# Kernel tuning notes

Hardware: AMD Instinct MI355X
Metric: run time of the kernel (lower is better)

## Reference

```python
import jax, jax.numpy as jnp
import numpy as np

B, T, D = 2, 512, 512
NUM_SCALES, MIN_S, MAX_S = 10, 0.01, 1.0
SCALES_NP = np.logspace(np.log10(MIN_S), np.log10(MAX_S), NUM_SCALES)


def _golay():
    # extended Golay (24,12) generator exactly as in _initialize_golay_code
    G = np.zeros((12, 24), np.float32)
    for i in range(12):
        G[i, i] = 1.0
        for j in range(11):
            G[i, 12 + j] = (i + j) % 2
        G[i, 23] = G[i, :23].sum() % 2
    return jnp.asarray(G)

GOLAY = _golay()  # [12,24]


def setup_inputs() -> dict:
    key = jax.random.key(0)
    ks = jax.random.split(key, 6)
    return {
        'token_ids': jax.random.randint(ks[0], (B, T), 0, 1000000, dtype=jnp.int32),
        'resonances': jax.random.uniform(ks[1], (D,), minval=1.0, maxval=50.0, dtype=jnp.float32),
        'emb_scales': jnp.ones((D,), jnp.float32),
        'emb_shifts': jnp.zeros((D,), jnp.float32),
        'emb_norm': jnp.ones((1,), jnp.float32),
        'scale_weights': jnp.ones((NUM_SCALES,), jnp.float32),
        'fractal_bias': jnp.zeros((1,), jnp.float32),
        'frac_norm': jnp.ones((1,), jnp.float32),
        'W_enc': jax.random.normal(ks[2], (D, 24), jnp.float32) / np.float32(np.sqrt(D)),
        'b_enc': jnp.zeros((24,), jnp.float32),
        'W_dec': jax.random.normal(ks[3], (24, D), jnp.float32) / np.float32(np.sqrt(24)),
        'b_dec': jnp.zeros((D,), jnp.float32),
        'ecc_strength': jnp.full((1,), 0.1, jnp.float32),
        'energy_preservation': jnp.ones((1,), jnp.float32),
    }


def _fractal_dimension(signal, scale_weights, fractal_bias, frac_norm):
    # differentiable box-counting (GenuineFractalAnalyzer.compute_fractal_dimension)
    input_energy = jnp.linalg.norm(signal)
    s = signal.reshape(-1)  # [N]
    s = (s - s.min()) / (s.max() - s.min() + 1e-8)
    counts = []
    for scale_np in SCALES_NP:
        nb = int(round(1.0 / scale_np))  # static per scale: 100 ... 1
        edges = jnp.linspace(0.0, 1.0, nb + 1)
        lo, hi = edges[:-1][:, None], edges[1:][:, None]  # [nb,1]
        # vectorized over boxes instead of python loop over boxes
        in_box = jax.nn.sigmoid(10.0 * (s[None, :] - lo)) * jax.nn.sigmoid(10.0 * (hi - s[None, :]))  # [nb,N]
        occ = in_box.sum(axis=1)  # [nb]
        counts.append(jax.nn.sigmoid(occ - 0.5).sum())
    box_counts = jnp.stack(counts)  # [NUM_SCALES]
    weighted = box_counts * jax.nn.softmax(scale_weights)
    scales = jnp.asarray(SCALES_NP, jnp.float32)
    log_x = jnp.log(1.0 / scales)
    log_y = jnp.log(weighted + 1e-8)
    n = np.float32(NUM_SCALES)
    sx, sy = log_x.sum(), log_y.sum()
    sxy, sx2 = (log_x * log_y).sum(), (log_x ** 2).sum()
    slope = (n * sxy - sx * sy) / (n * sx2 - sx ** 2 + 1e-8)
    fd = jnp.clip(-slope + fractal_bias, 1.0, 2.5)  # [1]
    out_energy = jnp.linalg.norm(fd)
    return fd * frac_norm * input_energy / out_energy


def reference(token_ids, resonances, emb_scales, emb_shifts, emb_norm, scale_weights,
              fractal_bias, frac_norm, W_enc, b_enc, W_dec, b_dec, ecc_strength,
              energy_preservation):
    # --- GenuineEmbedding.batch_encode (vectorized over B,T,D) ---
    token_value = (token_ids % 1000000).astype(jnp.float32) / 1e6  # [B,T]
    pos = jnp.arange(T, dtype=jnp.float32)  # [T]
    angle = resonances[None, None, :] * (token_value[:, :, None] + pos[None, :, None])  # [B,T,D]
    c, sn = jnp.cos(angle), jnp.sin(angle)
    comp = c * (1.0 + sn) + sn * sn
    emb = comp * emb_scales + emb_shifts
    tok_norm = jnp.linalg.norm(emb, axis=-1, keepdims=True)
    emb = jnp.where(tok_norm > 0, emb * emb_norm / tok_norm, emb)

    # --- GenuineLeechLattice.encode_to_lattice ---
    ecc = ecc_strength[0]
    ep = energy_preservation[0]
    e_in = jnp.linalg.norm(emb, axis=-1, keepdims=True)  # b t 1
    proj = emb @ W_enc + b_enc  # [B,T,24]
    golay_enc = jnp.einsum('btl,kl->btk', proj, GOLAY)  # [B,T,12]
    latt = jnp.round(golay_enc / ecc) * ecc
    e_out = jnp.linalg.norm(latt, axis=-1, keepdims=True)
    latt = latt * (e_in / (e_out + 1e-8)) * ep

    # --- GenuineLeechLattice.decode_from_lattice ---
    e_in2 = jnp.linalg.norm(latt, axis=-1, keepdims=True)
    golay_dec = jnp.einsum('btk,kl->btl', latt, GOLAY)  # [B,T,24]
    corrected = jnp.where(jnp.abs(golay_dec) > ecc, golay_dec, 0.0)
    res = corrected @ W_dec + b_dec  # [B,T,D]
    e_out2 = jnp.linalg.norm(res, axis=-1, keepdims=True)
    res = res * (e_in2 / (e_out2 + 1e-8)) * ep

    # --- GenuineFractalAnalyzer on the corrected signal, then modulate ---
    fd = _fractal_dimension(res, scale_weights, fractal_bias, frac_norm)  # [1]
    return res * fd
```

## Files before the change

### kernel.cpp

```cpp
#include <hip/hip_runtime.h>
#include <math.h>

#define NT   1024
#define TT   512
#define DD   512


__device__ __forceinline__ float np_pairwise512(const float* x, int tid) {
    float r = 0.0f;
    if (tid < 32) {
        const int b = tid >> 3, j = tid & 7;
        const float* p = x + 128 * b + j;
        r = p[0];
        #pragma unroll
        for (int i = 1; i < 16; i++) r = __fadd_rn(r, p[8 * i]);
    }
    r = __fadd_rn(r, __shfl_down(r, 1, 64));
    r = __fadd_rn(r, __shfl_down(r, 2, 64));
    r = __fadd_rn(r, __shfl_down(r, 4, 64));
    r = __fadd_rn(r, __shfl_down(r, 8, 64));
    r = __fadd_rn(r, __shfl_down(r, 16, 64));
    return r;
}

__device__ __forceinline__ float np_pairwise12(const float* a) {
    float r = __fadd_rn(__fadd_rn(__fadd_rn(a[0], a[1]), __fadd_rn(a[2], a[3])),
                        __fadd_rn(__fadd_rn(a[4], a[5]), __fadd_rn(a[6], a[7])));
    r = __fadd_rn(r, a[8]);
    r = __fadd_rn(r, a[9]);
    r = __fadd_rn(r, a[10]);
    r = __fadd_rn(r, a[11]);
    return r;
}

__global__ __launch_bounds__(512, 6) void token_kernel(
    const int*   __restrict__ token_ids,
    const float* __restrict__ resonances,
    const float* __restrict__ emb_scales,
    const float* __restrict__ emb_shifts,
    const float* __restrict__ emb_norm,
    const float* __restrict__ W_enc,
    const float* __restrict__ b_enc,
    const float* __restrict__ W_dec,
    const float* __restrict__ b_dec,
    const float* __restrict__ ecc_p,
    const float* __restrict__ ep_p,
    float*       __restrict__ out,
    double*      __restrict__ partials)
{
    const int tok  = blockIdx.x;
    const int t    = tok % TT;
    const int tid  = threadIdx.x;
    const int lane = tid & 63;
    const int wave = tid >> 6;

    __shared__ float  sh_w[DD * 24];
    __shared__ float  sh_e[DD];
    __shared__ float  sh_x[DD];
    __shared__ float  sh_c[24];
    __shared__ float  sh_sc[4];
    __shared__ double sh_red[8];

    {
        const float4* src = (const float4*)W_enc;
        float4*       dst = (float4*)sh_w;
        #pragma unroll
        for (int i = 0; i < 6; i++)
            dst[tid + 512 * i] = src[tid + 512 * i];
    }

    const float ecc   = ecc_p[0];
    const float ep    = ep_p[0];
    const float enorm = emb_norm[0];

    const int   idv  = token_ids[tok];
    const float tv   = __fdiv_rn((float)idv, 1000000.0f);
    const float base = __fadd_rn(tv, (float)t);

    float e0;
    {
        const float a0 = __fmul_rn(resonances[tid], base);
        double s0d, c0d;
        sincos((double)a0, &s0d, &c0d);
        const float s0 = (float)s0d, c0 = (float)c0d;
        const float comp0 = __fadd_rn(__fmul_rn(c0, __fadd_rn(1.0f, s0)), __fmul_rn(s0, s0));
        e0 = __fadd_rn(__fmul_rn(comp0, emb_scales[tid]), emb_shifts[tid]);
    }
    sh_x[tid] = __fmul_rn(e0, e0);
    __syncthreads();

    float ps = np_pairwise512(sh_x, tid);
    if (tid == 0) sh_sc[0] = __fsqrt_rn(ps);
    __syncthreads();
    const float tok_norm = sh_sc[0];
    if (tok_norm > 0.0f)
        e0 = __fdiv_rn(__fmul_rn(e0, enorm), tok_norm);
    sh_e[tid] = e0;
    sh_x[tid] = __fmul_rn(e0, e0);
    __syncthreads();

    ps = np_pairwise512(sh_x, tid);
    const float e_in = __fsqrt_rn(ps);

    if (wave == 0) {
        float p = 0.0f;
        if (lane < 24) {
            float acc = 0.0f;
            #pragma unroll 8
            for (int d = 0; d < DD; d++)
                acc = fmaf(sh_e[d], sh_w[d * 24 + lane], acc);
            p = __fadd_rn(acc, b_enc[lane]);
        }

        float latt = 0.0f;
        {
            const int k = lane;
            float g = p;
            #pragma unroll
            for (int l = 12; l < 23; l++) {
                const float v = __shfl(p, l, 64);
                if ((k + l) & 1) g = __fadd_rn(g, v);
            }
            const float v23 = __shfl(p, 23, 64);
            if (k & 1) g = __fadd_rn(g, v23);
            latt = __fmul_rn(rintf(__fdiv_rn(g, ecc)), ecc);
        }

        float lt[12];
        #pragma unroll
        for (int k = 0; k < 12; k++) lt[k] = __shfl(latt, k, 64);
        float m1;
        {
            float sq[12];
            #pragma unroll
            for (int k = 0; k < 12; k++) sq[k] = __fmul_rn(lt[k], lt[k]);
            const float e_out = __fsqrt_rn(np_pairwise12(sq));
            m1 = __fdiv_rn(e_in, __fadd_rn(e_out, 1e-8f));
        }
        m1 = __shfl(m1, 0, 64);
        float lv[12];
        #pragma unroll
        for (int k = 0; k < 12; k++) lv[k] = __fmul_rn(__fmul_rn(lt[k], m1), ep);
        if (lane == 0) {
            float sq[12];
            #pragma unroll
            for (int k = 0; k < 12; k++) sq[k] = __fmul_rn(lv[k], lv[k]);
            sh_sc[2] = __fsqrt_rn(np_pairwise12(sq));
        }

        if (lane < 24) {
            const int l = lane;
            float g;
            if (l < 12) {
                g = lv[l];
            } else if (l < 23) {
                g = 0.0f;
                #pragma unroll
                for (int k = 0; k < 12; k++)
                    if ((k + l) & 1) g = __fadd_rn(g, lv[k]);
            } else {
                g = 0.0f;
                for (int k = 1; k < 12; k += 2) g = __fadd_rn(g, lv[k]);
            }
            sh_c[l] = (fabsf(g) > ecc) ? g : 0.0f;
        }
    }
    __syncthreads();

    float r0 = 0.0f;
    #pragma unroll
    for (int l = 0; l < 24; l++)
        r0 = fmaf(sh_c[l], W_dec[l * DD + tid], r0);
    r0 = __fadd_rn(r0, b_dec[tid]);
    sh_x[tid] = __fmul_rn(r0, r0);
    __syncthreads();
    ps = np_pairwise512(sh_x, tid);
    if (tid == 0) sh_sc[3] = __fsqrt_rn(ps);
    __syncthreads();

    const float m2 = __fdiv_rn(sh_sc[2], __fadd_rn(sh_sc[3], 1e-8f));
    const float f0 = __fmul_rn(__fmul_rn(r0, m2), ep);
    out[tok * DD + tid] = f0;

    double v4 = (double)f0 * (double)f0;
    for (int off = 32; off > 0; off >>= 1) v4 += __shfl_down(v4, off, 64);
    if (lane == 0) sh_red[wave] = v4;
    __syncthreads();
    if (tid == 0) {
        double s = sh_red[0];
        #pragma unroll
        for (int w = 1; w < 8; w++) s += sh_red[w];
        partials[tok] = s;
    }
}

__global__ __launch_bounds__(256) void scale_kernel(
    float*        __restrict__ out,
    const double* __restrict__ partials,
    const float*  __restrict__ frac_norm)
{
    const int tid = threadIdx.x;
    __shared__ double sh[4];
    __shared__ float sh_factor;
    double s = 0.0;
    #pragma unroll
    for (int i = 0; i < 4; i++) s += partials[tid + 256 * i];
    for (int off = 32; off > 0; off >>= 1) s += __shfl_down(s, off, 64);
    if ((tid & 63) == 0) sh[tid >> 6] = s;
    __syncthreads();
    if (tid == 0)
        sh_factor = (float)((double)frac_norm[0] * sqrt(sh[0] + sh[1] + sh[2] + sh[3]));
    __syncthreads();
    const float factor = sh_factor;

    const int i = blockIdx.x * blockDim.x + tid;
    float4 r = ((const float4*)out)[i];
    r.x = __fmul_rn(r.x, factor);
    r.y = __fmul_rn(r.y, factor);
    r.z = __fmul_rn(r.z, factor);
    r.w = __fmul_rn(r.w, factor);
    ((float4*)out)[i] = r;
}

extern "C" void kernel_launch(void* const* d_in, const int* in_sizes, int n_in,
                              void* d_out, int out_size, void* d_ws, size_t ws_size,
                              hipStream_t stream)
{
    const int*   token_ids  = (const int*)  d_in[0];
    const float* resonances = (const float*)d_in[1];
    const float* emb_scales = (const float*)d_in[2];
    const float* emb_shifts = (const float*)d_in[3];
    const float* emb_norm   = (const float*)d_in[4];
    const float* frac_norm  = (const float*)d_in[7];
    const float* W_enc      = (const float*)d_in[8];
    const float* b_enc      = (const float*)d_in[9];
    const float* W_dec      = (const float*)d_in[10];
    const float* b_dec      = (const float*)d_in[11];
    const float* ecc        = (const float*)d_in[12];
    const float* ep         = (const float*)d_in[13];

    double* partials = (double*)d_ws;

    token_kernel<<<NT, 512, 0, stream>>>(token_ids, resonances, emb_scales, emb_shifts,
                                         emb_norm, W_enc, b_enc, W_dec, b_dec, ecc, ep,
                                         (float*)d_out, partials);
    scale_kernel<<<(NT * DD) / 1024, 256, 0, stream>>>((float*)d_out, partials, frac_norm);
}
```

Measured before the change: 102.9 us.

## Process four tokens per 1024-thread block to share the W_enc LDS tile

Each block now handles four tokens, with 256 threads per token and two embedding dimensions per thread. The 48KB W_enc shared-memory load is amortised over four tokens instead of one, cutting global-to-LDS traffic and the number of block launches fourfold. The cost is one large block per CU, which relies on four concurrent encode waves for latency hiding. The per-token double sum of squares now pairs two elements per thread before the shuffle, which slightly changes the reduction order.

```diff
diff --git a/kernel.cpp b/kernel.cpp
--- a/kernel.cpp
+++ b/kernel.cpp
@@ -6,10 +6,10 @@
 #define DD   512
 
 
-__device__ __forceinline__ float np_pairwise512(const float* x, int tid) {
+__device__ __forceinline__ float np_pairwise512(const float* x, int htid) {
     float r = 0.0f;
-    if (tid < 32) {
-        const int b = tid >> 3, j = tid & 7;
+    if (htid < 32) {
+        const int b = htid >> 3, j = htid & 7;
         const float* p = x + 128 * b + j;
         r = p[0];
         #pragma unroll
@@ -33,7 +33,7 @@
     return r;
 }
 
-__global__ __launch_bounds__(512, 6) void token_kernel(
+__global__ __launch_bounds__(1024, 4) void token_kernel(
     const int*   __restrict__ token_ids,
     const float* __restrict__ resonances,
     const float* __restrict__ emb_scales,
@@ -48,25 +48,27 @@
     float*       __restrict__ out,
     double*      __restrict__ partials)
 {
-    const int tok  = blockIdx.x;
+    const int tid  = threadIdx.x;
+    const int q    = tid >> 8;
+    const int htid = tid & 255;
+    const int tok  = blockIdx.x * 4 + q;
     const int t    = tok % TT;
-    const int tid  = threadIdx.x;
-    const int lane = tid & 63;
-    const int wave = tid >> 6;
+    const int w4   = htid >> 6;
+    const int hlane = htid & 63;
 
     __shared__ float  sh_w[DD * 24];
-    __shared__ float  sh_e[DD];
-    __shared__ float  sh_x[DD];
-    __shared__ float  sh_c[24];
-    __shared__ float  sh_sc[4];
-    __shared__ double sh_red[8];
+    __shared__ float  sh_e[4][DD];
+    __shared__ float  sh_x[4][DD];
+    __shared__ float  sh_c[4][24];
+    __shared__ float  sh_sc[4][4];
+    __shared__ double sh_red[4][4];
 
     {
         const float4* src = (const float4*)W_enc;
         float4*       dst = (float4*)sh_w;
         #pragma unroll
-        for (int i = 0; i < 6; i++)
-            dst[tid + 512 * i] = src[tid + 512 * i];
+        for (int i = 0; i < 3; i++)
+            dst[tid + 1024 * i] = src[tid + 1024 * i];
     }
 
     const float ecc   = ecc_p[0];
@@ -77,44 +79,54 @@
     const float tv   = __fdiv_rn((float)idv, 1000000.0f);
     const float base = __fadd_rn(tv, (float)t);
 
-    float e0;
+    const int d0 = htid, d1 = htid + 256;
+    float e0, e1;
     {
-        const float a0 = __fmul_rn(resonances[tid], base);
-        double s0d, c0d;
+        const float a0 = __fmul_rn(resonances[d0], base);
+        const float a1 = __fmul_rn(resonances[d1], base);
+        double s0d, c0d, s1d, c1d;
         sincos((double)a0, &s0d, &c0d);
+        sincos((double)a1, &s1d, &c1d);
         const float s0 = (float)s0d, c0 = (float)c0d;
+        const float s1 = (float)s1d, c1 = (float)c1d;
         const float comp0 = __fadd_rn(__fmul_rn(c0, __fadd_rn(1.0f, s0)), __fmul_rn(s0, s0));
-        e0 = __fadd_rn(__fmul_rn(comp0, emb_scales[tid]), emb_shifts[tid]);
-    }
-    sh_x[tid] = __fmul_rn(e0, e0);
-    __syncthreads();
-
-    float ps = np_pairwise512(sh_x, tid);
-    if (tid == 0) sh_sc[0] = __fsqrt_rn(ps);
-    __syncthreads();
-    const float tok_norm = sh_sc[0];
-    if (tok_norm > 0.0f)
+        const float comp1 = __fadd_rn(__fmul_rn(c1, __fadd_rn(1.0f, s1)), __fmul_rn(s1, s1));
+        e0 = __fadd_rn(__fmul_rn(comp0, emb_scales[d0]), emb_shifts[d0]);
+        e1 = __fadd_rn(__fmul_rn(comp1, emb_scales[d1]), emb_shifts[d1]);
+    }
+    sh_x[q][d0] = __fmul_rn(e0, e0);
+    sh_x[q][d1] = __fmul_rn(e1, e1);
+    __syncthreads();
+
+    float ps = np_pairwise512(sh_x[q], htid);
+    if (htid == 0) sh_sc[q][0] = __fsqrt_rn(ps);
+    __syncthreads();
+    const float tok_norm = sh_sc[q][0];
+    if (tok_norm > 0.0f) {
         e0 = __fdiv_rn(__fmul_rn(e0, enorm), tok_norm);
-    sh_e[tid] = e0;
-    sh_x[tid] = __fmul_rn(e0, e0);
-    __syncthreads();
-
-    ps = np_pairwise512(sh_x, tid);
+        e1 = __fdiv_rn(__fmul_rn(e1, enorm), tok_norm);
+    }
+    sh_e[q][d0] = e0; sh_e[q][d1] = e1;
+    sh_x[q][d0] = __fmul_rn(e0, e0);
+    sh_x[q][d1] = __fmul_rn(e1, e1);
+    __syncthreads();
+
+    ps = np_pairwise512(sh_x[q], htid);
     const float e_in = __fsqrt_rn(ps);
 
-    if (wave == 0) {
+    if (w4 == 0) {
         float p = 0.0f;
-        if (lane < 24) {
+        if (hlane < 24) {
             float acc = 0.0f;
             #pragma unroll 8
             for (int d = 0; d < DD; d++)
-                acc = fmaf(sh_e[d], sh_w[d * 24 + lane], acc);
-            p = __fadd_rn(acc, b_enc[lane]);
+                acc = fmaf(sh_e[q][d], sh_w[d * 24 + hlane], acc);
+            p = __fadd_rn(acc, b_enc[hlane]);
         }
 
         float latt = 0.0f;
         {
-            const int k = lane;
+            const int k = hlane;
             float g = p;
             #pragma unroll
             for (int l = 12; l < 23; l++) {
@@ -141,15 +153,15 @@
         float lv[12];
         #pragma unroll
         for (int k = 0; k < 12; k++) lv[k] = __fmul_rn(__fmul_rn(lt[k], m1), ep);
-        if (lane == 0) {
+        if (hlane == 0) {
             float sq[12];
             #pragma unroll
             for (int k = 0; k < 12; k++) sq[k] = __fmul_rn(lv[k], lv[k]);
-            sh_sc[2] = __fsqrt_rn(np_pairwise12(sq));
-        }
-
-        if (lane < 24) {
-            const int l = lane;
+            sh_sc[q][2] = __fsqrt_rn(np_pairwise12(sq));
+        }
+
+        if (hlane < 24) {
+            const int l = hlane;
             float g;
             if (l < 12) {
                 g = lv[l];
@@ -162,36 +174,39 @@
                 g = 0.0f;
                 for (int k = 1; k < 12; k += 2) g = __fadd_rn(g, lv[k]);
             }
-            sh_c[l] = (fabsf(g) > ecc) ? g : 0.0f;
-        }
-    }
-    __syncthreads();
-
-    float r0 = 0.0f;
+            sh_c[q][l] = (fabsf(g) > ecc) ? g : 0.0f;
+        }
+    }
+    __syncthreads();
+
+    float r0 = 0.0f, r1 = 0.0f;
     #pragma unroll
-    for (int l = 0; l < 24; l++)
-        r0 = fmaf(sh_c[l], W_dec[l * DD + tid], r0);
-    r0 = __fadd_rn(r0, b_dec[tid]);
-    sh_x[tid] = __fmul_rn(r0, r0);
-    __syncthreads();
-    ps = np_pairwise512(sh_x, tid);
-    if (tid == 0) sh_sc[3] = __fsqrt_rn(ps);
-    __syncthreads();
-
-    const float m2 = __fdiv_rn(sh_sc[2], __fadd_rn(sh_sc[3], 1e-8f));
+    for (int l = 0; l < 24; l++) {
+        const float cl = sh_c[q][l];
+        r0 = fmaf(cl, W_dec[l * DD + d0], r0);
+        r1 = fmaf(cl, W_dec[l * DD + d1], r1);
+    }
+    r0 = __fadd_rn(r0, b_dec[d0]);
+    r1 = __fadd_rn(r1, b_dec[d1]);
+    sh_x[q][d0] = __fmul_rn(r0, r0);
+    sh_x[q][d1] = __fmul_rn(r1, r1);
+    __syncthreads();
+    ps = np_pairwise512(sh_x[q], htid);
+    if (htid == 0) sh_sc[q][3] = __fsqrt_rn(ps);
+    __syncthreads();
+
+    const float m2 = __fdiv_rn(sh_sc[q][2], __fadd_rn(sh_sc[q][3], 1e-8f));
     const float f0 = __fmul_rn(__fmul_rn(r0, m2), ep);
-    out[tok * DD + tid] = f0;
-
-    double v4 = (double)f0 * (double)f0;
+    const float f1 = __fmul_rn(__fmul_rn(r1, m2), ep);
+    out[tok * DD + d0] = f0;
+    out[tok * DD + d1] = f1;
+
+    double v4 = (double)f0 * (double)f0 + (double)f1 * (double)f1;
     for (int off = 32; off > 0; off >>= 1) v4 += __shfl_down(v4, off, 64);
-    if (lane == 0) sh_red[wave] = v4;
-    __syncthreads();
-    if (tid == 0) {
-        double s = sh_red[0];
-        #pragma unroll
-        for (int w = 1; w < 8; w++) s += sh_red[w];
-        partials[tok] = s;
-    }
+    if (hlane == 0) sh_red[q][w4] = v4;
+    __syncthreads();
+    if (htid == 0)
+        partials[tok] = sh_red[q][0] + sh_red[q][1] + sh_red[q][2] + sh_red[q][3];
 }
 
 __global__ __launch_bounds__(256) void scale_kernel(
@@ -241,8 +256,9 @@
 
     double* partials = (double*)d_ws;
 
-    token_kernel<<<NT, 512, 0, stream>>>(token_ids, resonances, emb_scales, emb_shifts,
-                                         emb_norm, W_enc, b_enc, W_dec, b_dec, ecc, ep,
-                                         (float*)d_out, partials);
+    token_kernel<<<NT / 4, 1024, 0, stream>>>(token_ids, resonances, emb_scales,
+                                              emb_shifts, emb_norm, W_enc, b_enc,
+                                              W_dec, b_dec, ecc, ep,
+                                              (float*)d_out, partials);
     scale_kernel<<<(NT * DD) / 1024, 256, 0, stream>>>((float*)d_out, partials, frac_norm);
 }
```

New measurement: 95.31 us, median of 2. 7.4% less time.
